# Kernel optimization log

Hardware: AMD Instinct MI355X
Metric: run time of the kernel (lower is better)

## Reference

```python
import jax, jax.numpy as jnp
import numpy as np

NUM_USER = 24000
NUM_ITEM = 8000
DIM_E = 64
V_DIM = 2048
T_DIM = 384
TOPK = 10
N_UI_LAYERS = 2
LAMBDA = 0.9
N_INTER = 400000


def _build_sim(x):
    xn = x / jnp.linalg.norm(x, axis=-1, keepdims=True)
    return xn @ xn.T


def _knn_sym(sim, topk):
    # top-k per row -> sparse graph with symmetric (D^-1/2 A D^-1/2) normalization
    n = sim.shape[0]
    val, ind = jax.lax.top_k(sim, topk)            # [n, k]
    row = jnp.repeat(jnp.arange(n), topk)
    w = val.reshape(-1)
    col = ind.reshape(-1)
    deg = jax.ops.segment_sum(w, row, num_segments=n)
    dis = jnp.where(deg > 0, deg ** -0.5, 0.0)     # inf -> 0 as in torch masked_fill
    return col, dis[row] * w * dis[col]


def setup_inputs() -> dict:
    key = jax.random.key(0)
    ks = jax.random.split(key, 12)
    user_emb = jax.random.normal(ks[0], (NUM_USER, DIM_E), jnp.float32) * 0.1
    item_emb = jax.random.normal(ks[1], (NUM_ITEM, DIM_E), jnp.float32) * 0.1
    v_feat = jax.random.normal(ks[2], (NUM_ITEM, V_DIM), jnp.float32)
    t_feat = jax.random.normal(ks[3], (NUM_ITEM, T_DIM), jnp.float32)
    W_v = jax.random.normal(ks[4], (V_DIM, DIM_E), jnp.float32) * (1.0 / np.sqrt(V_DIM))
    b_v = jnp.zeros((DIM_E,), jnp.float32)
    W_t = jax.random.normal(ks[5], (T_DIM, DIM_E), jnp.float32) * (1.0 / np.sqrt(T_DIM))
    b_t = jnp.zeros((DIM_E,), jnp.float32)
    Wq1 = jax.random.normal(ks[6], (DIM_E, DIM_E), jnp.float32) * (1.0 / np.sqrt(DIM_E))
    bq1 = jnp.zeros((DIM_E,), jnp.float32)
    wq2 = jax.random.normal(ks[7], (DIM_E,), jnp.float32) * (1.0 / np.sqrt(DIM_E))
    # bipartite user-item interaction edges, symmetrized (as in __init__)
    u = jax.random.randint(ks[8], (N_INTER,), 0, NUM_USER)
    it = jax.random.randint(ks[9], (N_INTER,), 0, NUM_ITEM) + NUM_USER
    ei = jnp.stack([u, it])
    edge_index = jnp.concatenate([ei, ei[::-1]], axis=1)  # [2, 2*N_INTER]
    # original (frozen) multimodal KNN graphs built from raw features at init
    orig_img_cols, orig_img_w = _knn_sym(_build_sim(v_feat), TOPK)
    orig_txt_cols, orig_txt_w = _knn_sym(_build_sim(t_feat), TOPK)
    return {"user_emb": user_emb, "item_emb": item_emb, "v_feat": v_feat,
            "t_feat": t_feat, "W_v": W_v, "b_v": b_v, "W_t": W_t, "b_t": b_t,
            "Wq1": Wq1, "bq1": bq1, "wq2": wq2,
            "orig_img_w": orig_img_w, "orig_txt_w": orig_txt_w,
            "edge_index": edge_index,
            "orig_img_cols": orig_img_cols, "orig_txt_cols": orig_txt_cols}


def reference(user_emb, item_emb, v_feat, t_feat, W_v, b_v, W_t, b_t,
              Wq1, bq1, wq2, orig_img_w, orig_txt_w,
              edge_index, orig_img_cols, orig_txt_cols):
    n_user, n_item = user_emb.shape[0], item_emb.shape[0]
    # modality projections
    image_feats = v_feat @ W_v + b_v
    text_feats = t_feat @ W_t + b_t
    # fresh KNN graphs from projected features (build_item_graph=True path)
    img_cols, img_w = _knn_sym(_build_sim(image_feats), TOPK)
    txt_cols, txt_w = _knn_sym(_build_sim(text_feats), TOPK)
    row = jnp.repeat(jnp.arange(n_item), TOPK)

    def fused_spmm(cols_new, w_new, cols_orig, w_orig, x):
        # (1-lam)*A_new + lam*A_orig, applied as a single sparse matmul
        rows = jnp.concatenate([row, row])
        cols = jnp.concatenate([cols_new, cols_orig])
        w = jnp.concatenate([(1.0 - LAMBDA) * w_new,
                             LAMBDA * jax.lax.stop_gradient(w_orig)])
        return jax.ops.segment_sum(w[:, None] * x[cols], rows, num_segments=n_item)

    # NOTE: source bug reproduced - mm_layers loop always re-reads item_embedding,
    # so effective propagation depth is 1 regardless of mm_layers.
    image_item = fused_spmm(img_cols, img_w, orig_img_cols, orig_img_w, item_emb)
    text_item = fused_spmm(txt_cols, txt_w, orig_txt_cols, orig_txt_w, item_emb)

    def q(x):
        return jnp.tanh(x @ Wq1 + bq1) @ wq2  # [n_item]

    att = jnp.stack([q(image_item), q(text_item)], axis=-1)  # [n_item, 2]
    wgt = jax.nn.softmax(att, axis=-1)
    h = wgt[:, :1] * image_item + wgt[:, 1:] * text_item

    # user-item GCN propagation with sym degree normalization
    ego = jnp.concatenate([user_emb, item_emb], axis=0)
    n = ego.shape[0]
    r, c = edge_index[0], edge_index[1]
    deg = jax.ops.segment_sum(jnp.ones_like(r, dtype=ego.dtype), r, num_segments=n)
    dis = jnp.where(deg > 0, deg ** -0.5, 0.0)
    norm = dis[r] * dis[c]
    embs = [ego]
    for _ in range(N_UI_LAYERS):
        ego = jax.ops.segment_sum(norm[:, None] * ego[c], r, num_segments=n)
        embs.append(ego)
    all_emb = jnp.mean(jnp.stack(embs, axis=1), axis=1)
    u_g, i_g = all_emb[:n_user], all_emb[n_user:]
    h_norm = h / jnp.maximum(jnp.linalg.norm(h, axis=1, keepdims=True), 1e-12)
    i_g = i_g + h_norm
    return jnp.concatenate([u_g, i_g], axis=0)
```

## Files before the change

kernel.cpp:

```cpp
#include <hip/hip_runtime.h>
#include <math.h>

#define N_USER 24000
#define N_ITEM 8000
#define N_NODE 32000
#define N_EDGE 800000
#define NJC    16
#define JCH    512

typedef __attribute__((ext_vector_type(8))) short bf16x8;
typedef __attribute__((ext_vector_type(4))) float f32x4;

__device__ __forceinline__ float wred_sum(float v) {
#pragma unroll
  for (int off = 32; off; off >>= 1) v += __shfl_xor(v, off, 64);
  return v;
}

__device__ __forceinline__ unsigned short f2bf(float f) {
  unsigned int u = __float_as_uint(f);
  unsigned int r = (u + 0x7fffu + ((u >> 16) & 1u)) >> 16;
  return (unsigned short)r;
}
__device__ __forceinline__ float bf2f(unsigned short h) {
  return __uint_as_float(((unsigned int)h) << 16);
}

__device__ __forceinline__ unsigned int umx(unsigned int a, unsigned int b) { return a > b ? a : b; }
__device__ __forceinline__ unsigned int umn(unsigned int a, unsigned int b) { return a < b ? a : b; }

__device__ __forceinline__ float key_val(unsigned int k) {
  return ((float)(int)(k >> 13) - 131080.0f) * (1.0f / 131072.0f);
}
__device__ __forceinline__ int key_idx(unsigned int k) {
  return 8191 - (int)(k & 8191u);
}

#define ASTR 132
#define NB_G 693
__global__ __launch_bounds__(256) void k_gemm_count(
    const float* __restrict__ Xi, const float* __restrict__ Wi,
    const float* __restrict__ Xt, const float* __restrict__ Wt,
    float* __restrict__ Pi, float* __restrict__ Pt,
    const int* __restrict__ r, int* __restrict__ degi)
{
  __shared__ float As[32 * ASTR];
  __shared__ float Bs[32 * 64];
  const int tid = threadIdx.x;
  const int b = blockIdx.x;
  if (b >= NB_G) {
    int e = (b - NB_G) * 256 + tid;
    atomicAdd(&degi[r[e]], 1);
    return;
  }
  const int m0 = (b % 63) * 128;
  const int cy = b / 63;
  const float* X; const float* W; float* out; int K, kc0, Klen;
  if (cy < 8) { X = Xi; W = Wi; K = 2048; Klen = 256; kc0 = cy * 256;
                out = Pi + (size_t)cy * N_ITEM * 64; }
  else        { X = Xt; W = Wt; K = 384;  Klen = 128; kc0 = (cy - 8) * 128;
                out = Pt + (size_t)(cy - 8) * N_ITEM * 64; }
  const int tr = tid >> 4, tc = tid & 15;
  float acc[8][4] = {};
  for (int k0 = kc0; k0 < kc0 + Klen; k0 += 32) {
    __syncthreads();
#pragma unroll
    for (int lq = 0; lq < 4; ++lq) {
      int u = tid + lq * 256;
      int rr = u >> 3, kq = u & 7;
      int row = m0 + rr; if (row > N_ITEM - 1) row = N_ITEM - 1;
      float4 a = *(const float4*)(X + (size_t)row * K + k0 + kq * 4);
      As[(kq * 4 + 0) * ASTR + rr] = a.x;
      As[(kq * 4 + 1) * ASTR + rr] = a.y;
      As[(kq * 4 + 2) * ASTR + rr] = a.z;
      As[(kq * 4 + 3) * ASTR + rr] = a.w;
    }
#pragma unroll
    for (int lq = 0; lq < 2; ++lq) {
      int u = tid + lq * 256;
      int kb = u >> 4, nq = u & 15;
      *(float4*)(Bs + kb * 64 + nq * 4) =
          *(const float4*)(W + (size_t)(k0 + kb) * 64 + nq * 4);
    }
    __syncthreads();
#pragma unroll
    for (int k = 0; k < 32; ++k) {
      float4 a0 = *(const float4*)(As + k * ASTR + tr * 8);
      float4 a1 = *(const float4*)(As + k * ASTR + tr * 8 + 4);
      float4 b4 = *(const float4*)(Bs + k * 64 + tc * 4);
      float av[8] = {a0.x, a0.y, a0.z, a0.w, a1.x, a1.y, a1.z, a1.w};
      float bv[4] = {b4.x, b4.y, b4.z, b4.w};
#pragma unroll
      for (int ri = 0; ri < 8; ++ri)
#pragma unroll
        for (int ci = 0; ci < 4; ++ci) acc[ri][ci] += av[ri] * bv[ci];
    }
  }
#pragma unroll
  for (int ri = 0; ri < 8; ++ri) {
    int row = m0 + tr * 8 + ri;
    if (row < N_ITEM) {
      float4 o;
      o.x = acc[ri][0]; o.y = acc[ri][1]; o.z = acc[ri][2]; o.w = acc[ri][3];
      *(float4*)(out + (size_t)row * 64 + tc * 4) = o;
    }
  }
}

__global__ __launch_bounds__(256) void norm_dual(
    const float* __restrict__ Pi, const float* __restrict__ bi,
    unsigned short* __restrict__ Xhi, unsigned short* __restrict__ Xli,
    const float* __restrict__ Pt, const float* __restrict__ bt,
    unsigned short* __restrict__ Xht, unsigned short* __restrict__ Xlt)
{
  const float* P; const float* bias; unsigned short *Xh, *Xl; int nk;
  if (blockIdx.y == 0) { P = Pi; bias = bi; Xh = Xhi; Xl = Xli; nk = 8; }
  else                 { P = Pt; bias = bt; Xh = Xht; Xl = Xlt; nk = 3; }
  int row = blockIdx.x * 4 + (threadIdx.x >> 6);
  int lane = threadIdx.x & 63;
  size_t o = (size_t)row * 64 + lane;
  float v = bias[lane];
  for (int q = 0; q < nk; ++q) v += P[(size_t)q * N_ITEM * 64 + o];
  float ss = wred_sum(v * v);
  float xn = v * rsqrtf(ss);
  unsigned short hi = f2bf(xn);
  Xh[o] = hi;
  Xl[o] = f2bf(xn - bf2f(hi));
}

#define NB_SIM 2016
__global__ __launch_bounds__(256) void k_sim_scan(
    const unsigned short* __restrict__ Xhi, const unsigned short* __restrict__ Xli,
    const unsigned short* __restrict__ Xht, const unsigned short* __restrict__ Xlt,
    unsigned int* __restrict__ pk,
    const int* __restrict__ degi, int* __restrict__ offs, float* __restrict__ disui)
{
  __shared__ char lds[2 * 2 * 32 * 128];
  const int tid = threadIdx.x;

  if (blockIdx.x == 0) {
    int* stot  = (int*)lds;
    int* sbase = (int*)lds + 512;
    int lane = tid & 63, w = tid >> 6;
    for (int k = 0; k < 125; ++k) {
      int c = w * 125 + k;
      int d = degi[c * 64 + lane];
      int s = d;
#pragma unroll
      for (int off = 32; off; off >>= 1) s += __shfl_xor(s, off, 64);
      if (lane == 0) stot[c] = s;
    }
    __syncthreads();
    if (w == 0) {
      int run = 0;
      for (int r = 0; r < 8; ++r) {
        int idx = r * 64 + lane;
        int v = (idx < 500) ? stot[idx] : 0;
        int p = v;
#pragma unroll
        for (int off = 1; off < 64; off <<= 1) {
          int n = __shfl_up(p, off, 64);
          if (lane >= off) p += n;
        }
        if (idx < 500) sbase[idx] = run + p - v;
        run += __shfl(p, 63, 64);
      }
    }
    __syncthreads();
    for (int k = 0; k < 125; ++k) {
      int c = w * 125 + k;
      int i = c * 64 + lane;
      int d = degi[i];
      int p = d;
#pragma unroll
      for (int off = 1; off < 64; off <<= 1) {
        int n = __shfl_up(p, off, 64);
        if (lane >= off) p += n;
      }
      offs[i] = sbase[c] + p - d;
      disui[i] = d > 0 ? rsqrtf((float)d) : 0.f;
    }
    if (tid == 0) offs[N_NODE] = N_EDGE;
    return;
  }

  const int b = blockIdx.x - 1;
  const int bz = b / 1008;
  const int rem = b % 1008;
  const int by = rem / 63;
  const int bx = rem % 63;
  const unsigned short* Xh = bz ? Xht : Xhi;
  const unsigned short* Xl = bz ? Xlt : Xli;
  unsigned int* pkm = pk + (size_t)bz * N_ITEM * (NJC * 10);

  const int l = tid & 63;
  const int wid = tid >> 6;
  const int ib = bx * 128 + wid * 32;
  const int jc = by * JCH;
  const bool lastc = (jc + JCH > N_ITEM);

  bf16x8 bh[2][2], bl[2][2];
#pragma unroll
  for (int s = 0; s < 2; ++s) {
    int irow = ib + s * 16 + (l & 15);
    if (irow > N_ITEM - 1) irow = N_ITEM - 1;
    int ksl = (l >> 4) * 8;
#pragma unroll
    for (int kh = 0; kh < 2; ++kh) {
      bh[s][kh] = *(const bf16x8*)(Xh + (size_t)irow * 64 + kh * 32 + ksl);
      bl[s][kh] = *(const bf16x8*)(Xl + (size_t)irow * 64 + kh * 32 + ksl);
    }
  }

  unsigned int K0[10], K1[10];
#pragma unroll
  for (int t = 0; t < 10; ++t) { K0[t] = 0u; K1[t] = 0u; }

  auto stage = [&](int bb, int p) {
    int row = tid >> 3, cb = (tid & 7) * 16;
    int gr = jc + p * 32 + row;
    if (gr > N_ITEM - 1) gr = N_ITEM - 1;
    int4 vh = *(const int4*)(Xh + (size_t)gr * 64 + (cb >> 1));
    int4 vl = *(const int4*)(Xl + (size_t)gr * 64 + (cb >> 1));
    int bo = (row * 128 + cb) ^ ((row & 7) << 4);
    *(int4*)(lds + bb * 8192 + bo) = vh;
    *(int4*)(lds + bb * 8192 + 4096 + bo) = vl;
  };

#define EPI(MASKED)                                                            \
  _Pragma("unroll")                                                            \
  for (int s = 0; s < 2; ++s) {                                                \
    unsigned int* K = s ? K1 : K0;                                             \
    _Pragma("unroll")                                                          \
    for (int t = 0; t < 2; ++t) {                                              \
      _Pragma("unroll")                                                        \
      for (int r = 0; r < 4; ++r) {                                            \
        float f = acc[t][s][r];                                                \
        unsigned int v19 = (unsigned int)(int)(f * 131072.0f + 131080.0f);     \
        unsigned int key = (v19 << 13) | (unsigned int)jinv[t * 4 + r];        \
        if (MASKED) key = (jinv[t * 4 + r] >= 192) ? key : 0u;                 \
        _Pragma("unroll")                                                      \
        for (int q = 0; q < 10; ++q) {                                         \
          unsigned int mn = umn(K[q], key);                                    \
          K[q] = umx(K[q], key);                                               \
          key = mn;                                                            \
        }                                                                      \
      }                                                                        \
    }                                                                          \
  }

  stage(0, 0);
  int cur = 0;
  for (int p = 0; p < 16; ++p) {
    __syncthreads();
    if (p < 15) stage(cur ^ 1, p + 1);
    const char* ldsH = lds + cur * 8192;
    const char* ldsL = ldsH + 4096;
    f32x4 acc[2][2] = {};
#pragma unroll
    for (int t = 0; t < 2; ++t) {
      int jr = t * 16 + (l & 15);
      int sw = (jr & 7) << 4;
      int rb = jr * 128 + ((l >> 4) << 4);
      bf16x8 ah0 = *(const bf16x8*)(ldsH + (rb ^ sw));
      bf16x8 ah1 = *(const bf16x8*)(ldsH + ((rb + 64) ^ sw));
      bf16x8 al0 = *(const bf16x8*)(ldsL + (rb ^ sw));
      bf16x8 al1 = *(const bf16x8*)(ldsL + ((rb + 64) ^ sw));
#pragma unroll
      for (int s = 0; s < 2; ++s) {
        acc[t][s] = __builtin_amdgcn_mfma_f32_16x16x32_bf16(ah0, bh[s][0], acc[t][s], 0, 0, 0);
        acc[t][s] = __builtin_amdgcn_mfma_f32_16x16x32_bf16(ah1, bh[s][1], acc[t][s], 0, 0, 0);
        acc[t][s] = __builtin_amdgcn_mfma_f32_16x16x32_bf16(ah0, bl[s][0], acc[t][s], 0, 0, 0);
        acc[t][s] = __builtin_amdgcn_mfma_f32_16x16x32_bf16(ah1, bl[s][1], acc[t][s], 0, 0, 0);
        acc[t][s] = __builtin_amdgcn_mfma_f32_16x16x32_bf16(al0, bh[s][0], acc[t][s], 0, 0, 0);
        acc[t][s] = __builtin_amdgcn_mfma_f32_16x16x32_bf16(al1, bh[s][1], acc[t][s], 0, 0, 0);
      }
    }
    const int jg0 = jc + p * 32 + ((l >> 4) << 2);
    int jinv[8];
#pragma unroll
    for (int t = 0; t < 2; ++t)
#pragma unroll
      for (int r = 0; r < 4; ++r)
        jinv[t * 4 + r] = 8191 - (jg0 + t * 16 + r);
    if (!lastc) { EPI(false) } else { EPI(true) }
    cur ^= 1;
  }
#undef EPI

#pragma unroll
  for (int s = 0; s < 2; ++s) {
    unsigned int* K = s ? K1 : K0;
    unsigned int kv[10];
#pragma unroll
    for (int t = 0; t < 10; ++t) {
      unsigned int m = K[0];
      m = umx(m, (unsigned int)__shfl_xor((int)m, 16, 64));
      m = umx(m, (unsigned int)__shfl_xor((int)m, 32, 64));
      bool own = (K[0] == m);
#pragma unroll
      for (int q2 = 0; q2 < 9; ++q2) K[q2] = own ? K[q2 + 1] : K[q2];
      K[9] = own ? 0u : K[9];
      kv[t] = m;
    }
    int i = ib + s * 16 + (l & 15);
    if (l < 16 && i < N_ITEM) {
      size_t base = ((size_t)i * NJC + by) * 10;
#pragma unroll
      for (int t = 0; t < 10; ++t) pkm[base + t] = kv[t];
    }
  }
}

#define NB_M 4000
__global__ __launch_bounds__(256) void k_merge_fill(
    const unsigned int* __restrict__ pk,
    float* __restrict__ tv_i, int* __restrict__ tc_i, float* __restrict__ dis_i,
    float* __restrict__ tv_t, int* __restrict__ tc_t, float* __restrict__ dis_t,
    const int* __restrict__ r, const int* __restrict__ c,
    const int* __restrict__ offs, int* __restrict__ cursor, int* __restrict__ csr)
{
  int b = blockIdx.x;
  int tid = threadIdx.x;
  if (b >= NB_M) {
    int e = (b - NB_M) * 256 + tid;
    int rr = r[e];
    int pos = offs[rr] + atomicAdd(&cursor[rr], 1);
    csr[pos] = c[e];
    return;
  }
  int my = b / 2000, mx = b % 2000;
  float* tv; int* tc; float* dis;
  if (my == 0) { tv = tv_i; tc = tc_i; dis = dis_i; }
  else         { tv = tv_t; tc = tc_t; dis = dis_t; }
  int lane = tid & 63;
  int row = mx * 4 + (tid >> 6);
  size_t base = (size_t)my * N_ITEM * (NJC * 10) + (size_t)row * (NJC * 10);
  unsigned int k0 = pk[base + lane];
  unsigned int k1 = pk[base + 64 + lane];
  unsigned int k2 = (lane < 32) ? pk[base + 128 + lane] : 0u;
  float deg = 0.f, keepv = 0.f; int keepc = 0;
  for (int t = 0; t < 10; ++t) {
    unsigned int m = umx(umx(k0, k1), k2);
#pragma unroll
    for (int off = 32; off; off >>= 1)
      m = umx(m, (unsigned int)__shfl_xor((int)m, off, 64));
    deg += key_val(m);
    if (k0 == m) k0 = 0u;
    else if (k1 == m) k1 = 0u;
    else if (k2 == m) k2 = 0u;
    if (lane == t) { keepv = key_val(m); keepc = key_idx(m); }
  }
  if (lane < 10) { tv[(size_t)row * 10 + lane] = keepv; tc[(size_t)row * 10 + lane] = keepc; }
  if (lane == 0) dis[row] = deg > 0.f ? rsqrtf(deg) : 0.f;
}

#define NB_S 2000
__global__ __launch_bounds__(256) void k_spmm_prop1(
    const float* __restrict__ tv_i, const int* __restrict__ tc_i, const float* __restrict__ dis_i,
    const float* __restrict__ ow_i, const int* __restrict__ oc_i,
    const float* __restrict__ tv_t, const int* __restrict__ tc_t, const float* __restrict__ dis_t,
    const float* __restrict__ ow_t, const int* __restrict__ oc_t,
    const float* __restrict__ item_emb,
    const float* __restrict__ Wq1, const float* __restrict__ bq1,
    const float* __restrict__ wq2, float* __restrict__ hn,
    const float* __restrict__ ue, float* __restrict__ E1,
    const int* __restrict__ offs, const int* __restrict__ csr,
    const float* __restrict__ dis)
{
  __shared__ float Wlds[64 * 64];
  __shared__ float sm[4][2][64];
  int tid = threadIdx.x;
  int lane = tid & 63, wid = tid >> 6;
  int b = blockIdx.x;
  if (b >= NB_S) {
    int row = (b - NB_S) * 4 + wid;
    int q = lane >> 3, c8 = lane & 7;
    float4 acc0 = make_float4(0.f, 0.f, 0.f, 0.f);
    float4 acc1 = make_float4(0.f, 0.f, 0.f, 0.f);
    int e0 = offs[row], e1 = offs[row + 1];
    for (int e = e0 + q; e < e1; e += 8) {
      int cc = csr[e];
      const float* src = cc < N_USER ? ue + (size_t)cc * 64
                                     : item_emb + (size_t)(cc - N_USER) * 64;
      float4 v0 = *(const float4*)(src + c8 * 8);
      float4 v1 = *(const float4*)(src + c8 * 8 + 4);
      float d = dis[cc];
      acc0.x += d * v0.x; acc0.y += d * v0.y; acc0.z += d * v0.z; acc0.w += d * v0.w;
      acc1.x += d * v1.x; acc1.y += d * v1.y; acc1.z += d * v1.z; acc1.w += d * v1.w;
    }
#pragma unroll
    for (int off = 8; off <= 32; off <<= 1) {
      acc0.x += __shfl_xor(acc0.x, off, 64);
      acc0.y += __shfl_xor(acc0.y, off, 64);
      acc0.z += __shfl_xor(acc0.z, off, 64);
      acc0.w += __shfl_xor(acc0.w, off, 64);
      acc1.x += __shfl_xor(acc1.x, off, 64);
      acc1.y += __shfl_xor(acc1.y, off, 64);
      acc1.z += __shfl_xor(acc1.z, off, 64);
      acc1.w += __shfl_xor(acc1.w, off, 64);
    }
    if (q == 0) {
      float dr = dis[row];
      acc0.x *= dr; acc0.y *= dr; acc0.z *= dr; acc0.w *= dr;
      acc1.x *= dr; acc1.y *= dr; acc1.z *= dr; acc1.w *= dr;
      *(float4*)(E1 + (size_t)row * 64 + c8 * 8) = acc0;
      *(float4*)(E1 + (size_t)row * 64 + c8 * 8 + 4) = acc1;
    }
    return;
  }
  int row = b * 4 + wid;
#pragma unroll
  for (int s = 0; s < 4; ++s) {
    int idx = tid + s * 256;
    ((float4*)Wlds)[idx] = ((const float4*)Wq1)[idx];
  }
  float a0 = 0.f, a1 = 0.f;
  {
    float disr = dis_i[row];
#pragma unroll
    for (int t = 0; t < 10; ++t) {
      int c = tc_i[(size_t)row * 10 + t];
      a0 += 0.1f * disr * tv_i[(size_t)row * 10 + t] * dis_i[c] * item_emb[(size_t)c * 64 + lane];
    }
#pragma unroll
    for (int t = 0; t < 10; ++t) {
      int c = oc_i[(size_t)row * 10 + t];
      a0 += 0.9f * ow_i[(size_t)row * 10 + t] * item_emb[(size_t)c * 64 + lane];
    }
  }
  {
    float disr = dis_t[row];
#pragma unroll
    for (int t = 0; t < 10; ++t) {
      int c = tc_t[(size_t)row * 10 + t];
      a1 += 0.1f * disr * tv_t[(size_t)row * 10 + t] * dis_t[c] * item_emb[(size_t)c * 64 + lane];
    }
#pragma unroll
    for (int t = 0; t < 10; ++t) {
      int c = oc_t[(size_t)row * 10 + t];
      a1 += 0.9f * ow_t[(size_t)row * 10 + t] * item_emb[(size_t)c * 64 + lane];
    }
  }
  sm[wid][0][lane] = a0;
  sm[wid][1][lane] = a1;
  __syncthreads();
  float y0 = bq1[lane], y1 = bq1[lane];
  for (int k = 0; k < 64; ++k) {
    float w = Wlds[k * 64 + lane];
    y0 += sm[wid][0][k] * w;
    y1 += sm[wid][1][k] * w;
  }
  float wq = wq2[lane];
  float s0 = wred_sum(tanhf(y0) * wq);
  float s1 = wred_sum(tanhf(y1) * wq);
  float mx = fmaxf(s0, s1);
  float e0 = expf(s0 - mx), e1 = expf(s1 - mx);
  float inv = 1.f / (e0 + e1);
  float h = (e0 * inv) * a0 + (e1 * inv) * a1;
  float n2 = wred_sum(h * h);
  float nrm = fmaxf(sqrtf(n2), 1e-12f);
  hn[(size_t)row * 64 + lane] = h / nrm;
}

__global__ __launch_bounds__(256) void k_prop2(
    const float* __restrict__ in, const float* __restrict__ ue,
    const float* __restrict__ ie, float* __restrict__ out,
    const int* __restrict__ offs, const int* __restrict__ csr,
    const float* __restrict__ dis, const float* __restrict__ hn)
{
  int tid = threadIdx.x;
  int lane = tid & 63, wid = tid >> 6;
  int row = blockIdx.x * 4 + wid;
  int q = lane >> 3, c8 = lane & 7;
  float4 acc0 = make_float4(0.f, 0.f, 0.f, 0.f);
  float4 acc1 = make_float4(0.f, 0.f, 0.f, 0.f);
  int e0 = offs[row], e1 = offs[row + 1];
  for (int e = e0 + q; e < e1; e += 8) {
    int cc = csr[e];
    const float* src = in + (size_t)cc * 64;
    float4 v0 = *(const float4*)(src + c8 * 8);
    float4 v1 = *(const float4*)(src + c8 * 8 + 4);
    float d = dis[cc];
    acc0.x += d * v0.x; acc0.y += d * v0.y; acc0.z += d * v0.z; acc0.w += d * v0.w;
    acc1.x += d * v1.x; acc1.y += d * v1.y; acc1.z += d * v1.z; acc1.w += d * v1.w;
  }
#pragma unroll
  for (int off = 8; off <= 32; off <<= 1) {
    acc0.x += __shfl_xor(acc0.x, off, 64);
    acc0.y += __shfl_xor(acc0.y, off, 64);
    acc0.z += __shfl_xor(acc0.z, off, 64);
    acc0.w += __shfl_xor(acc0.w, off, 64);
    acc1.x += __shfl_xor(acc1.x, off, 64);
    acc1.y += __shfl_xor(acc1.y, off, 64);
    acc1.z += __shfl_xor(acc1.z, off, 64);
    acc1.w += __shfl_xor(acc1.w, off, 64);
  }
  if (q == 0) {
    float dr = dis[row];
    acc0.x *= dr; acc0.y *= dr; acc0.z *= dr; acc0.w *= dr;
    acc1.x *= dr; acc1.y *= dr; acc1.z *= dr; acc1.w *= dr;
    const float* egop = (row < N_USER) ? ue + (size_t)row * 64
                                       : ie + (size_t)(row - N_USER) * 64;
    float4 eg0 = *(const float4*)(egop + c8 * 8);
    float4 eg1 = *(const float4*)(egop + c8 * 8 + 4);
    float4 l10 = *(const float4*)(in + (size_t)row * 64 + c8 * 8);
    float4 l11 = *(const float4*)(in + (size_t)row * 64 + c8 * 8 + 4);
    float4 o0, o1;
    o0.x = (eg0.x + l10.x + acc0.x) * (1.f / 3.f);
    o0.y = (eg0.y + l10.y + acc0.y) * (1.f / 3.f);
    o0.z = (eg0.z + l10.z + acc0.z) * (1.f / 3.f);
    o0.w = (eg0.w + l10.w + acc0.w) * (1.f / 3.f);
    o1.x = (eg1.x + l11.x + acc1.x) * (1.f / 3.f);
    o1.y = (eg1.y + l11.y + acc1.y) * (1.f / 3.f);
    o1.z = (eg1.z + l11.z + acc1.z) * (1.f / 3.f);
    o1.w = (eg1.w + l11.w + acc1.w) * (1.f / 3.f);
    if (row >= N_USER) {
      const float* hp = hn + (size_t)(row - N_USER) * 64;
      float4 h0 = *(const float4*)(hp + c8 * 8);
      float4 h1 = *(const float4*)(hp + c8 * 8 + 4);
      o0.x += h0.x; o0.y += h0.y; o0.z += h0.z; o0.w += h0.w;
      o1.x += h1.x; o1.y += h1.y; o1.z += h1.z; o1.w += h1.w;
    }
    *(float4*)(out + (size_t)row * 64 + c8 * 8) = o0;
    *(float4*)(out + (size_t)row * 64 + c8 * 8 + 4) = o1;
  }
}

extern "C" void kernel_launch(void* const* d_in, const int* in_sizes, int n_in,
                              void* d_out, int out_size, void* d_ws, size_t ws_size,
                              hipStream_t stream)
{
  (void)in_sizes; (void)n_in; (void)out_size; (void)ws_size;
  const float* user_emb = (const float*)d_in[0];
  const float* item_emb = (const float*)d_in[1];
  const float* v_feat   = (const float*)d_in[2];
  const float* t_feat   = (const float*)d_in[3];
  const float* W_v      = (const float*)d_in[4];
  const float* b_v      = (const float*)d_in[5];
  const float* W_t      = (const float*)d_in[6];
  const float* b_t      = (const float*)d_in[7];
  const float* Wq1      = (const float*)d_in[8];
  const float* bq1      = (const float*)d_in[9];
  const float* wq2      = (const float*)d_in[10];
  const float* ow_i     = (const float*)d_in[11];
  const float* ow_t     = (const float*)d_in[12];
  const int*   eidx     = (const int*)d_in[13];
  const int*   oc_i     = (const int*)d_in[14];
  const int*   oc_t     = (const int*)d_in[15];
  float* out = (float*)d_out;

  char* wp = (char*)d_ws;
  auto alloc = [&](size_t bytes) -> void* {
    void* p = (void*)wp;
    wp += (bytes + 255) & ~(size_t)255;
    return p;
  };
  char* regionA = (char*)alloc((size_t)8 * N_ITEM * 64 * 4 + 1024);
  char* regionB = (char*)alloc((size_t)N_NODE * 64 * 4 + 1024);
  float* Pp_i = (float*)regionA;
  float* Pp_t = (float*)regionB;
  unsigned int* pk = (unsigned int*)regionA;
  float* E1 = (float*)regionB;

  unsigned short* Xhi = (unsigned short*)alloc((size_t)N_ITEM * 64 * 2);
  unsigned short* Xli = (unsigned short*)alloc((size_t)N_ITEM * 64 * 2);
  unsigned short* Xht = (unsigned short*)alloc((size_t)N_ITEM * 64 * 2);
  unsigned short* Xlt = (unsigned short*)alloc((size_t)N_ITEM * 64 * 2);
  float* tv_i  = (float*)alloc((size_t)N_ITEM * 10 * 4);
  int*   tc_i  = (int*)  alloc((size_t)N_ITEM * 10 * 4);
  float* dis_i = (float*)alloc((size_t)N_ITEM * 4);
  float* tv_t  = (float*)alloc((size_t)N_ITEM * 10 * 4);
  int*   tc_t  = (int*)  alloc((size_t)N_ITEM * 10 * 4);
  float* dis_t = (float*)alloc((size_t)N_ITEM * 4);
  float* hn    = (float*)alloc((size_t)N_ITEM * 64 * 4);
  int*   degcur= (int*)  alloc((size_t)2 * N_NODE * 4);
  int*   degi  = degcur;
  int*   curs  = degcur + N_NODE;
  int*   offs  = (int*)  alloc((size_t)(N_NODE + 1) * 4);
  float* disui = (float*)alloc((size_t)N_NODE * 4);
  int*   csr   = (int*)  alloc((size_t)N_EDGE * 4);

  hipMemsetAsync(degcur, 0, (size_t)2 * N_NODE * 4, stream);
  k_gemm_count<<<NB_G + 3125, 256, 0, stream>>>(v_feat, W_v, t_feat, W_t, Pp_i, Pp_t,
                                                eidx, degi);
  norm_dual<<<dim3(2000, 2), 256, 0, stream>>>(Pp_i, b_v, Xhi, Xli, Pp_t, b_t, Xht, Xlt);
  k_sim_scan<<<NB_SIM + 1, 256, 0, stream>>>(Xhi, Xli, Xht, Xlt, pk, degi, offs, disui);
  k_merge_fill<<<NB_M + 3125, 256, 0, stream>>>(pk, tv_i, tc_i, dis_i, tv_t, tc_t, dis_t,
                                                eidx, eidx + N_EDGE, offs, curs, csr);
  k_spmm_prop1<<<NB_S + 8000, 256, 0, stream>>>(tv_i, tc_i, dis_i, ow_i, oc_i,
                                                tv_t, tc_t, dis_t, ow_t, oc_t,
                                                item_emb, Wq1, bq1, wq2, hn,
                                                user_emb, E1, offs, csr, disui);
  k_prop2<<<8000, 256, 0, stream>>>(E1, user_emb, item_emb, out, offs, csr, disui, hn);
}
```

Baseline: 302.6 us.

## Move feature projection GEMM to bf16 split-precision MFMA with fewer K-splits

Result: no change. 304.0 us (+0.5%).

```diff
diff --git a/kernel.cpp b/kernel.cpp
--- a/kernel.cpp
+++ b/kernel.cpp
@@ -36,16 +36,18 @@
   return 8191 - (int)(k & 8191u);
 }
 
-#define ASTR 132
-#define NB_G 693
+#define NB_G 378
 __global__ __launch_bounds__(256) void k_gemm_count(
     const float* __restrict__ Xi, const float* __restrict__ Wi,
     const float* __restrict__ Xt, const float* __restrict__ Wt,
     float* __restrict__ Pi, float* __restrict__ Pt,
     const int* __restrict__ r, int* __restrict__ degi)
 {
-  __shared__ float As[32 * ASTR];
-  __shared__ float Bs[32 * 64];
+  __shared__ char lds2[24576];
+  char* ldsXH = lds2;
+  char* ldsXL = lds2 + 8192;
+  char* ldsWH = lds2 + 16384;
+  char* ldsWL = lds2 + 20480;
   const int tid = threadIdx.x;
   const int b = blockIdx.x;
   if (b >= NB_G) {
@@ -55,56 +57,89 @@
   }
   const int m0 = (b % 63) * 128;
   const int cy = b / 63;
-  const float* X; const float* W; float* out; int K, kc0, Klen;
-  if (cy < 8) { X = Xi; W = Wi; K = 2048; Klen = 256; kc0 = cy * 256;
+  const float* X; const float* W; float* out; int K, kc0, ksteps;
+  if (cy < 4) { X = Xi; W = Wi; K = 2048; kc0 = cy * 512; ksteps = 16;
                 out = Pi + (size_t)cy * N_ITEM * 64; }
-  else        { X = Xt; W = Wt; K = 384;  Klen = 128; kc0 = (cy - 8) * 128;
-                out = Pt + (size_t)(cy - 8) * N_ITEM * 64; }
-  const int tr = tid >> 4, tc = tid & 15;
-  float acc[8][4] = {};
-  for (int k0 = kc0; k0 < kc0 + Klen; k0 += 32) {
+  else        { X = Xt; W = Wt; K = 384;  kc0 = (cy - 4) * 192; ksteps = 6;
+                out = Pt + (size_t)(cy - 4) * N_ITEM * 64; }
+  const int l = tid & 63;
+  const int wid = tid >> 6;
+  f32x4 acc[2][4] = {};
+
+  for (int ks = 0; ks < ksteps; ++ks) {
+    int k0 = kc0 + ks * 32;
     __syncthreads();
 #pragma unroll
     for (int lq = 0; lq < 4; ++lq) {
       int u = tid + lq * 256;
-      int rr = u >> 3, kq = u & 7;
-      int row = m0 + rr; if (row > N_ITEM - 1) row = N_ITEM - 1;
-      float4 a = *(const float4*)(X + (size_t)row * K + k0 + kq * 4);
-      As[(kq * 4 + 0) * ASTR + rr] = a.x;
-      As[(kq * 4 + 1) * ASTR + rr] = a.y;
-      As[(kq * 4 + 2) * ASTR + rr] = a.z;
-      As[(kq * 4 + 3) * ASTR + rr] = a.w;
+      int rr = u >> 3, q = u & 7;
+      int grow = m0 + rr; if (grow > N_ITEM - 1) grow = N_ITEM - 1;
+      float4 xv = *(const float4*)(X + (size_t)grow * K + k0 + q * 4);
+      unsigned short h0 = f2bf(xv.x), h1 = f2bf(xv.y), h2 = f2bf(xv.z), h3 = f2bf(xv.w);
+      unsigned int hA = ((unsigned int)h1 << 16) | h0;
+      unsigned int hB = ((unsigned int)h3 << 16) | h2;
+      unsigned short l0 = f2bf(xv.x - bf2f(h0)), l1 = f2bf(xv.y - bf2f(h1));
+      unsigned short l2 = f2bf(xv.z - bf2f(h2)), l3 = f2bf(xv.w - bf2f(h3));
+      unsigned int lA = ((unsigned int)l1 << 16) | l0;
+      unsigned int lB = ((unsigned int)l3 << 16) | l2;
+      int slot = q >> 1;
+      int bo = rr * 64 + ((slot ^ ((rr >> 1) & 3)) << 4) + (q & 1) * 8;
+      *(int2*)(ldsXH + bo) = make_int2((int)hA, (int)hB);
+      *(int2*)(ldsXL + bo) = make_int2((int)lA, (int)lB);
     }
 #pragma unroll
     for (int lq = 0; lq < 2; ++lq) {
       int u = tid + lq * 256;
-      int kb = u >> 4, nq = u & 15;
-      *(float4*)(Bs + kb * 64 + nq * 4) =
-          *(const float4*)(W + (size_t)(k0 + kb) * 64 + nq * 4);
+      int kb = u >> 4, nq = (u & 15) * 4;
+      float4 wv = *(const float4*)(W + (size_t)(k0 + kb) * 64 + nq);
+      int slot = kb >> 3, within = kb & 7;
+      float wa[4] = {wv.x, wv.y, wv.z, wv.w};
+#pragma unroll
+      for (int j = 0; j < 4; ++j) {
+        int n = nq + j;
+        unsigned short h = f2bf(wa[j]);
+        unsigned short lo = f2bf(wa[j] - bf2f(h));
+        int bo = n * 64 + ((slot ^ ((n >> 1) & 3)) << 4) + within * 2;
+        *(unsigned short*)(ldsWH + bo) = h;
+        *(unsigned short*)(ldsWL + bo) = lo;
+      }
     }
     __syncthreads();
-#pragma unroll
-    for (int k = 0; k < 32; ++k) {
-      float4 a0 = *(const float4*)(As + k * ASTR + tr * 8);
-      float4 a1 = *(const float4*)(As + k * ASTR + tr * 8 + 4);
-      float4 b4 = *(const float4*)(Bs + k * 64 + tc * 4);
-      float av[8] = {a0.x, a0.y, a0.z, a0.w, a1.x, a1.y, a1.z, a1.w};
-      float bv[4] = {b4.x, b4.y, b4.z, b4.w};
-#pragma unroll
-      for (int ri = 0; ri < 8; ++ri)
-#pragma unroll
-        for (int ci = 0; ci < 4; ++ci) acc[ri][ci] += av[ri] * bv[ci];
-    }
-  }
-#pragma unroll
-  for (int ri = 0; ri < 8; ++ri) {
-    int row = m0 + tr * 8 + ri;
-    if (row < N_ITEM) {
-      float4 o;
-      o.x = acc[ri][0]; o.y = acc[ri][1]; o.z = acc[ri][2]; o.w = acc[ri][3];
-      *(float4*)(out + (size_t)row * 64 + tc * 4) = o;
-    }
-  }
+    bf16x8 xh[2], xl[2], wh[4], wl[4];
+    int slot = l >> 4;
+#pragma unroll
+    for (int s = 0; s < 2; ++s) {
+      int rr = wid * 32 + s * 16 + (l & 15);
+      int bo = rr * 64 + ((slot ^ ((rr >> 1) & 3)) << 4);
+      xh[s] = *(const bf16x8*)(ldsXH + bo);
+      xl[s] = *(const bf16x8*)(ldsXL + bo);
+    }
+#pragma unroll
+    for (int nt = 0; nt < 4; ++nt) {
+      int n = nt * 16 + (l & 15);
+      int bo = n * 64 + ((slot ^ ((n >> 1) & 3)) << 4);
+      wh[nt] = *(const bf16x8*)(ldsWH + bo);
+      wl[nt] = *(const bf16x8*)(ldsWL + bo);
+    }
+#pragma unroll
+    for (int s = 0; s < 2; ++s)
+#pragma unroll
+      for (int nt = 0; nt < 4; ++nt) {
+        acc[s][nt] = __builtin_amdgcn_mfma_f32_16x16x32_bf16(xh[s], wh[nt], acc[s][nt], 0, 0, 0);
+        acc[s][nt] = __builtin_amdgcn_mfma_f32_16x16x32_bf16(xh[s], wl[nt], acc[s][nt], 0, 0, 0);
+        acc[s][nt] = __builtin_amdgcn_mfma_f32_16x16x32_bf16(xl[s], wh[nt], acc[s][nt], 0, 0, 0);
+      }
+  }
+#pragma unroll
+  for (int s = 0; s < 2; ++s)
+#pragma unroll
+    for (int nt = 0; nt < 4; ++nt)
+#pragma unroll
+      for (int r4 = 0; r4 < 4; ++r4) {
+        int gi = m0 + wid * 32 + s * 16 + ((l >> 4) << 2) + r4;
+        int gn = nt * 16 + (l & 15);
+        if (gi < N_ITEM) out[(size_t)gi * 64 + gn] = acc[s][nt][r4];
+      }
 }
 
 __global__ __launch_bounds__(256) void norm_dual(
@@ -114,8 +149,8 @@
     unsigned short* __restrict__ Xht, unsigned short* __restrict__ Xlt)
 {
   const float* P; const float* bias; unsigned short *Xh, *Xl; int nk;
-  if (blockIdx.y == 0) { P = Pi; bias = bi; Xh = Xhi; Xl = Xli; nk = 8; }
-  else                 { P = Pt; bias = bt; Xh = Xht; Xl = Xlt; nk = 3; }
+  if (blockIdx.y == 0) { P = Pi; bias = bi; Xh = Xhi; Xl = Xli; nk = 4; }
+  else                 { P = Pt; bias = bt; Xh = Xht; Xl = Xlt; nk = 2; }
   int row = blockIdx.x * 4 + (threadIdx.x >> 6);
   int lane = threadIdx.x & 63;
   size_t o = (size_t)row * 64 + lane;
```
